# Kernel tuning notes

Hardware: AMD Instinct MI355X
Metric: run time of the kernel (lower is better)

Reference implementation:

```python
import jax, jax.numpy as jnp
import numpy as np

IN_C = 128
OUT_C = 128
N_SAMPLES = 9
N_HEADS = 8
HEAD_C = OUT_C // N_HEADS
SCALE = HEAD_C ** (-0.5)
B, FH, FW = 4, 128, 128


def setup_inputs() -> dict:
    key = jax.random.key(0)
    ks = jax.random.split(key, 8)
    w_std = IN_C ** (-0.5)
    q = jax.random.normal(ks[0], (B, IN_C, FH, FW), dtype=jnp.float32)
    kv = jax.random.normal(ks[1], (B, IN_C, N_SAMPLES, FH * FW), dtype=jnp.float32)
    Wq = jax.random.normal(ks[2], (OUT_C, IN_C), dtype=jnp.float32) * w_std
    bq = jax.random.normal(ks[3], (OUT_C,), dtype=jnp.float32) * 0.01
    Wk = jax.random.normal(ks[4], (OUT_C, IN_C), dtype=jnp.float32) * w_std
    bk = jax.random.normal(ks[5], (OUT_C,), dtype=jnp.float32) * 0.01
    Wv = jax.random.normal(ks[6], (OUT_C, IN_C), dtype=jnp.float32) * w_std
    bv = jax.random.normal(ks[7], (OUT_C,), dtype=jnp.float32) * 0.01
    return {"q": q, "kv": kv, "Wq": Wq, "bq": bq, "Wk": Wk, "bk": bk, "Wv": Wv, "bv": bv}


def reference(q, kv, Wq, bq, Wk, bk, Wv, bv):
    b, c, fh, fw = q.shape
    d = fh * fw
    # 1x1 conv projections == channel matmuls
    qp = (jnp.einsum('oc,bchw->bohw', Wq, q) + bq[None, :, None, None])
    qp = qp.reshape(b * N_HEADS, HEAD_C, d)                       # [bH, hc, d]
    kp = (jnp.einsum('oc,bcsd->bosd', Wk, kv) + bk[None, :, None, None])
    kp = kp.reshape(b * N_HEADS, HEAD_C, N_SAMPLES, d)            # [bH, hc, s, d]
    vp = (jnp.einsum('oc,bcsd->bosd', Wv, kv) + bv[None, :, None, None])
    vp = vp.reshape(b * N_HEADS, HEAD_C, N_SAMPLES, d)
    # per-pixel attention over n_samples keys
    attn = jnp.einsum('bcd,bcsd->bsd', qp, kp) * SCALE            # [bH, s, d]
    attn = jax.nn.softmax(attn, axis=1)
    out = jnp.einsum('bsd,bcsd->bcd', attn, vp)                   # [bH, hc, d]
    return out.reshape(b, OUT_C, fh, fw)
```

## Files before the change

### kernel.cpp

```cpp
#include <hip/hip_runtime.h>

#define D_PIX 16384
#define NSMP  9
#define TP    64
#define RS    136

typedef __attribute__((ext_vector_type(8))) short s16x8;
typedef __attribute__((ext_vector_type(4))) short s16x4;
typedef __attribute__((ext_vector_type(4))) float f32x4;

__device__ __forceinline__ short f2b(float f) {
    union { float f; unsigned u; } c; c.f = f;
    unsigned r = (c.u + 0x7FFFu + ((c.u >> 16) & 1u)) >> 16;
    return (short)r;
}

__global__ __launch_bounds__(256, 2)
void deform_attn_kernel(const float* __restrict__ q,
                        const float* __restrict__ kv,
                        const float* __restrict__ Wq,
                        const float* __restrict__ bq,
                        const float* __restrict__ Wk,
                        const float* __restrict__ bk,
                        const float* __restrict__ Wv,
                        const float* __restrict__ bv,
                        float* __restrict__ out)
{
    __shared__ short ldsb[2][TP * RS];

    const int tid  = threadIdx.x;
    const int bid  = blockIdx.x;
    const int b    = bid >> 8;
    const int px0  = (bid & 255) * TP;
    const int lane = tid & 63;
    const int w    = tid >> 6;
    const int r    = lane & 15;
    const int quad = lane >> 4;

    const int pxb = (tid & 7) * 8;
    const int chb = (tid >> 3) * 4;

    f32x4 pref[4][2];
    auto stage_load = [&](const float* base, int chstride) {
        #pragma unroll
        for (int j = 0; j < 4; ++j) {
            const float* p = base + (long)(chb + j) * chstride + pxb;
            pref[j][0] = *(const f32x4*)p;
            pref[j][1] = *(const f32x4*)(p + 4);
        }
    };
    auto stage_write = [&](short* buf) {
        #pragma unroll
        for (int i = 0; i < 8; ++i) {
            s16x4 v4 = { f2b(pref[0][i >> 2][i & 3]), f2b(pref[1][i >> 2][i & 3]),
                         f2b(pref[2][i >> 2][i & 3]), f2b(pref[3][i >> 2][i & 3]) };
            *(s16x4*)(buf + (pxb + i) * RS + chb) = v4;
        }
    };
    auto load_bfrags = [&](const short* buf, int n, s16x8* bfr) {
        #pragma unroll
        for (int ks = 0; ks < 4; ++ks)
            bfr[ks] = *(const s16x8*)(buf + (n * 16 + r) * RS + ks * 32 + quad * 8);
    };
    auto load_wfrag = [&](const float* W, int o, int ks) -> s16x8 {
        const float* p = W + o * 128 + ks * 32 + quad * 8;
        f32x4 a = *(const f32x4*)p;
        f32x4 c = *(const f32x4*)(p + 4);
        s16x8 f = { f2b(a[0]), f2b(a[1]), f2b(a[2]), f2b(a[3]),
                    f2b(c[0]), f2b(c[1]), f2b(c[2]), f2b(c[3]) };
        return f;
    };

    s16x8 wkF[2][4], wvF[2][4];
    float bkf[2][4], bvf[2][4], bqf[2][4];
    #pragma unroll
    for (int m = 0; m < 2; ++m) {
        const int o = (2 * w + m) * 16 + r;
        #pragma unroll
        for (int ks = 0; ks < 4; ++ks) {
            wkF[m][ks] = load_wfrag(Wk, o, ks);
            wvF[m][ks] = load_wfrag(Wv, o, ks);
        }
        const int ob = (2 * w + m) * 16 + quad * 4;
        #pragma unroll
        for (int rr = 0; rr < 4; ++rr) {
            bqf[m][rr] = bq[ob + rr];
            bkf[m][rr] = bk[ob + rr];
            bvf[m][rr] = bv[ob + rr];
        }
    }

    float qp[2][4][4];
    float oacc[2][4][4];
    float lsum[2][4];
    #pragma unroll
    for (int m = 0; m < 2; ++m)
        #pragma unroll
        for (int n = 0; n < 4; ++n) {
            lsum[m][n] = 0.f;
            #pragma unroll
            for (int rr = 0; rr < 4; ++rr) oacc[m][n][rr] = 0.f;
        }

    const float* qbase  = q  + (long)(b * 128) * D_PIX + px0;
    const float* kvbase = kv + (long)(b * 128) * NSMP * D_PIX + px0;

    stage_load(qbase, D_PIX);
    stage_write(ldsb[0]);
    __syncthreads();

    stage_load(kvbase, NSMP * D_PIX);
    {
        s16x8 wqF[2][4];
        #pragma unroll
        for (int m = 0; m < 2; ++m) {
            const int o = (2 * w + m) * 16 + r;
            #pragma unroll
            for (int ks = 0; ks < 4; ++ks)
                wqF[m][ks] = load_wfrag(Wq, o, ks);
        }
        #pragma unroll
        for (int n = 0; n < 4; ++n) {
            s16x8 bfr[4];
            load_bfrags(ldsb[0], n, bfr);
            #pragma unroll
            for (int m = 0; m < 2; ++m) {
                f32x4 acc = {0.f, 0.f, 0.f, 0.f};
                #pragma unroll
                for (int ks = 0; ks < 4; ++ks)
                    acc = __builtin_amdgcn_mfma_f32_16x16x32_bf16(wqF[m][ks], bfr[ks], acc, 0, 0, 0);
                #pragma unroll
                for (int rr = 0; rr < 4; ++rr) qp[m][n][rr] = acc[rr] + bqf[m][rr];
            }
        }
    }
    stage_write(ldsb[1]);
    __syncthreads();

    for (int s = 0; s < NSMP; ++s) {
        if (s < NSMP - 1) stage_load(kvbase + (s + 1) * D_PIX, NSMP * D_PIX);
        const short* buf = ldsb[(s + 1) & 1];
        #pragma unroll
        for (int n = 0; n < 4; ++n) {
            s16x8 bfr[4];
            load_bfrags(buf, n, bfr);
            #pragma unroll
            for (int m = 0; m < 2; ++m) {
                f32x4 kacc = {0.f, 0.f, 0.f, 0.f};
                f32x4 vacc = {0.f, 0.f, 0.f, 0.f};
                #pragma unroll
                for (int ks = 0; ks < 4; ++ks) {
                    kacc = __builtin_amdgcn_mfma_f32_16x16x32_bf16(wkF[m][ks], bfr[ks], kacc, 0, 0, 0);
                    vacc = __builtin_amdgcn_mfma_f32_16x16x32_bf16(wvF[m][ks], bfr[ks], vacc, 0, 0, 0);
                }
                float pf = 0.f;
                #pragma unroll
                for (int rr = 0; rr < 4; ++rr) pf += qp[m][n][rr] * (kacc[rr] + bkf[m][rr]);
                pf += __shfl_xor(pf, 16, 64);
                pf += __shfl_xor(pf, 32, 64);
                const float e = __expf(pf * 0.25f);
                lsum[m][n] += e;
                #pragma unroll
                for (int rr = 0; rr < 4; ++rr) oacc[m][n][rr] += e * (vacc[rr] + bvf[m][rr]);
            }
        }
        if (s < NSMP - 1) stage_write(ldsb[s & 1]);
        __syncthreads();
    }

    #pragma unroll
    for (int m = 0; m < 2; ++m) {
        #pragma unroll
        for (int n = 0; n < 4; ++n) {
            const float inv = 1.f / lsum[m][n];
            #pragma unroll
            for (int rr = 0; rr < 4; ++rr) {
                const int o = (2 * w + m) * 16 + quad * 4 + rr;
                out[(long)(b * 128 + o) * D_PIX + px0 + n * 16 + r] = oacc[m][n][rr] * inv;
            }
        }
    }
}

extern "C" void kernel_launch(void* const* d_in, const int* in_sizes, int n_in,
                              void* d_out, int out_size, void* d_ws, size_t ws_size,
                              hipStream_t stream) {
    const float* q  = (const float*)d_in[0];
    const float* kv = (const float*)d_in[1];
    const float* Wq = (const float*)d_in[2];
    const float* bq = (const float*)d_in[3];
    const float* Wk = (const float*)d_in[4];
    const float* bk = (const float*)d_in[5];
    const float* Wv = (const float*)d_in[6];
    const float* bv = (const float*)d_in[7];
    float* out = (float*)d_out;

    dim3 grid(1024);
    dim3 block(256);
    hipLaunchKernelGGL(deform_attn_kernel, grid, block, 0, stream,
                       q, kv, Wq, bq, Wk, bk, Wv, bv, out);
}
```

Baseline: 459.3 us.

## Use 512-thread blocks with one head per wave and fold biases algebraically

Doubles the block to 512 threads so each of eight waves owns a single 16-channel head, which halves per-thread register state (weights, accumulators) and the staging load per thread. The key bias is folded into a per-pixel constant q·bk computed once, and the value bias is added after normalisation because the softmax weights sum to one. The LDS row stride changes to 132 to suit the new 2-channel writes. The aim is higher occupancy and better latency hiding, at the cost of more waves contending at each barrier and a possible change in LDS bank conflicts.

```diff
diff --git a/kernel.cpp b/kernel.cpp
--- a/kernel.cpp
+++ b/kernel.cpp
@@ -3,10 +3,9 @@
 #define D_PIX 16384
 #define NSMP  9
 #define TP    64
-#define RS    136
+#define RS    132
 
 typedef __attribute__((ext_vector_type(8))) short s16x8;
-typedef __attribute__((ext_vector_type(4))) short s16x4;
 typedef __attribute__((ext_vector_type(4))) float f32x4;
 
 __device__ __forceinline__ short f2b(float f) {
@@ -15,7 +14,7 @@
     return (short)r;
 }
 
-__global__ __launch_bounds__(256, 2)
+__global__ __launch_bounds__(512, 4)
 void deform_attn_kernel(const float* __restrict__ q,
                         const float* __restrict__ kv,
                         const float* __restrict__ Wq,
@@ -38,12 +37,12 @@
     const int quad = lane >> 4;
 
     const int pxb = (tid & 7) * 8;
-    const int chb = (tid >> 3) * 4;
+    const int chb = (tid >> 3) * 2;
 
-    f32x4 pref[4][2];
-    auto stage_load = [&](const float* base, int chstride) {
+    f32x4 pref[2][2];
+    auto stage_load = [&](const float* base, long chstride) {
         #pragma unroll
-        for (int j = 0; j < 4; ++j) {
+        for (int j = 0; j < 2; ++j) {
             const float* p = base + (long)(chb + j) * chstride + pxb;
             pref[j][0] = *(const f32x4*)p;
             pref[j][1] = *(const f32x4*)(p + 4);
@@ -52,9 +51,8 @@
     auto stage_write = [&](short* buf) {
         #pragma unroll
         for (int i = 0; i < 8; ++i) {
-            s16x4 v4 = { f2b(pref[0][i >> 2][i & 3]), f2b(pref[1][i >> 2][i & 3]),
-                         f2b(pref[2][i >> 2][i & 3]), f2b(pref[3][i >> 2][i & 3]) };
-            *(s16x4*)(buf + (pxb + i) * RS + chb) = v4;
+            short2 v = { f2b(pref[0][i >> 2][i & 3]), f2b(pref[1][i >> 2][i & 3]) };
+            *(short2*)(buf + (pxb + i) * RS + chb) = v;
         }
     };
     auto load_bfrags = [&](const short* buf, int n, s16x8* bfr) {
@@ -71,113 +69,102 @@
         return f;
     };
 
-    s16x8 wkF[2][4], wvF[2][4];
-    float bkf[2][4], bvf[2][4], bqf[2][4];
-    #pragma unroll
-    for (int m = 0; m < 2; ++m) {
-        const int o = (2 * w + m) * 16 + r;
-        #pragma unroll
-        for (int ks = 0; ks < 4; ++ks) {
-            wkF[m][ks] = load_wfrag(Wk, o, ks);
-            wvF[m][ks] = load_wfrag(Wv, o, ks);
-        }
-        const int ob = (2 * w + m) * 16 + quad * 4;
-        #pragma unroll
-        for (int rr = 0; rr < 4; ++rr) {
-            bqf[m][rr] = bq[ob + rr];
-            bkf[m][rr] = bk[ob + rr];
-            bvf[m][rr] = bv[ob + rr];
-        }
-    }
-
-    float qp[2][4][4];
-    float oacc[2][4][4];
-    float lsum[2][4];
-    #pragma unroll
-    for (int m = 0; m < 2; ++m)
-        #pragma unroll
-        for (int n = 0; n < 4; ++n) {
-            lsum[m][n] = 0.f;
-            #pragma unroll
-            for (int rr = 0; rr < 4; ++rr) oacc[m][n][rr] = 0.f;
-        }
-
     const float* qbase  = q  + (long)(b * 128) * D_PIX + px0;
     const float* kvbase = kv + (long)(b * 128) * NSMP * D_PIX + px0;
+    const long   kvstr  = (long)NSMP * D_PIX;
 
     stage_load(qbase, D_PIX);
     stage_write(ldsb[0]);
     __syncthreads();
 
-    stage_load(kvbase, NSMP * D_PIX);
+    stage_load(kvbase, kvstr);
+    float qp[4][4];
     {
-        s16x8 wqF[2][4];
+        const int o = w * 16 + r;
+        s16x8 wqF[4];
         #pragma unroll
-        for (int m = 0; m < 2; ++m) {
-            const int o = (2 * w + m) * 16 + r;
-            #pragma unroll
-            for (int ks = 0; ks < 4; ++ks)
-                wqF[m][ks] = load_wfrag(Wq, o, ks);
-        }
+        for (int ks = 0; ks < 4; ++ks) wqF[ks] = load_wfrag(Wq, o, ks);
+        const int ob = w * 16 + quad * 4;
         #pragma unroll
         for (int n = 0; n < 4; ++n) {
             s16x8 bfr[4];
             load_bfrags(ldsb[0], n, bfr);
+            f32x4 acc = {0.f, 0.f, 0.f, 0.f};
             #pragma unroll
-            for (int m = 0; m < 2; ++m) {
-                f32x4 acc = {0.f, 0.f, 0.f, 0.f};
-                #pragma unroll
-                for (int ks = 0; ks < 4; ++ks)
-                    acc = __builtin_amdgcn_mfma_f32_16x16x32_bf16(wqF[m][ks], bfr[ks], acc, 0, 0, 0);
-                #pragma unroll
-                for (int rr = 0; rr < 4; ++rr) qp[m][n][rr] = acc[rr] + bqf[m][rr];
-            }
+            for (int ks = 0; ks < 4; ++ks)
+                acc = __builtin_amdgcn_mfma_f32_16x16x32_bf16(wqF[ks], bfr[ks], acc, 0, 0, 0);
+            #pragma unroll
+            for (int rr = 0; rr < 4; ++rr) qp[n][rr] = acc[rr] + bq[ob + rr];
         }
     }
     stage_write(ldsb[1]);
+
+    s16x8 wkF[4], wvF[4];
+    float bvf[4], qb[4];
+    {
+        const int o = w * 16 + r;
+        #pragma unroll
+        for (int ks = 0; ks < 4; ++ks) {
+            wkF[ks] = load_wfrag(Wk, o, ks);
+            wvF[ks] = load_wfrag(Wv, o, ks);
+        }
+        const int ob = w * 16 + quad * 4;
+        float bkf[4];
+        #pragma unroll
+        for (int rr = 0; rr < 4; ++rr) { bkf[rr] = bk[ob + rr]; bvf[rr] = bv[ob + rr]; }
+        #pragma unroll
+        for (int n = 0; n < 4; ++n) {
+            qb[n] = 0.f;
+            #pragma unroll
+            for (int rr = 0; rr < 4; ++rr) qb[n] += qp[n][rr] * bkf[rr];
+        }
+    }
+
+    float oacc[4][4];
+    float lsum[4];
+    #pragma unroll
+    for (int n = 0; n < 4; ++n) {
+        lsum[n] = 0.f;
+        #pragma unroll
+        for (int rr = 0; rr < 4; ++rr) oacc[n][rr] = 0.f;
+    }
     __syncthreads();
 
     for (int s = 0; s < NSMP; ++s) {
-        if (s < NSMP - 1) stage_load(kvbase + (s + 1) * D_PIX, NSMP * D_PIX);
+        if (s < NSMP - 1) stage_load(kvbase + (s + 1) * D_PIX, kvstr);
         const short* buf = ldsb[(s + 1) & 1];
         #pragma unroll
         for (int n = 0; n < 4; ++n) {
             s16x8 bfr[4];
             load_bfrags(buf, n, bfr);
+            f32x4 kacc = {0.f, 0.f, 0.f, 0.f};
+            f32x4 vacc = {0.f, 0.f, 0.f, 0.f};
             #pragma unroll
-            for (int m = 0; m < 2; ++m) {
-                f32x4 kacc = {0.f, 0.f, 0.f, 0.f};
-                f32x4 vacc = {0.f, 0.f, 0.f, 0.f};
-                #pragma unroll
-                for (int ks = 0; ks < 4; ++ks) {
-                    kacc = __builtin_amdgcn_mfma_f32_16x16x32_bf16(wkF[m][ks], bfr[ks], kacc, 0, 0, 0);
-                    vacc = __builtin_amdgcn_mfma_f32_16x16x32_bf16(wvF[m][ks], bfr[ks], vacc, 0, 0, 0);
-                }
-                float pf = 0.f;
-                #pragma unroll
-                for (int rr = 0; rr < 4; ++rr) pf += qp[m][n][rr] * (kacc[rr] + bkf[m][rr]);
-                pf += __shfl_xor(pf, 16, 64);
-                pf += __shfl_xor(pf, 32, 64);
-                const float e = __expf(pf * 0.25f);
-                lsum[m][n] += e;
-                #pragma unroll
-                for (int rr = 0; rr < 4; ++rr) oacc[m][n][rr] += e * (vacc[rr] + bvf[m][rr]);
+            for (int ks = 0; ks < 4; ++ks) {
+                kacc = __builtin_amdgcn_mfma_f32_16x16x32_bf16(wkF[ks], bfr[ks], kacc, 0, 0, 0);
+                vacc = __builtin_amdgcn_mfma_f32_16x16x32_bf16(wvF[ks], bfr[ks], vacc, 0, 0, 0);
             }
+            float pf = qb[n];
+            #pragma unroll
+            for (int rr = 0; rr < 4; ++rr) pf += qp[n][rr] * kacc[rr];
+            pf += __shfl_xor(pf, 16, 64);
+            pf += __shfl_xor(pf, 32, 64);
+            const float e = __expf(pf * 0.25f);
+            lsum[n] += e;
+            #pragma unroll
+            for (int rr = 0; rr < 4; ++rr) oacc[n][rr] += e * vacc[rr];
         }
         if (s < NSMP - 1) stage_write(ldsb[s & 1]);
         __syncthreads();
     }
 
     #pragma unroll
-    for (int m = 0; m < 2; ++m) {
+    for (int n = 0; n < 4; ++n) {
+        const float inv = 1.f / lsum[n];
         #pragma unroll
-        for (int n = 0; n < 4; ++n) {
-            const float inv = 1.f / lsum[m][n];
-            #pragma unroll
-            for (int rr = 0; rr < 4; ++rr) {
-                const int o = (2 * w + m) * 16 + quad * 4 + rr;
-                out[(long)(b * 128 + o) * D_PIX + px0 + n * 16 + r] = oacc[m][n][rr] * inv;
-            }
+        for (int rr = 0; rr < 4; ++rr) {
+            const int o = w * 16 + quad * 4 + rr;
+            out[(long)(b * 128 + o) * D_PIX + px0 + n * 16 + r] = oacc[n][rr] * inv + bvf[rr];
         }
     }
 }
@@ -196,7 +183,7 @@
     float* out = (float*)d_out;
 
     dim3 grid(1024);
-    dim3 block(256);
+    dim3 block(512);
     hipLaunchKernelGGL(deform_attn_kernel, grid, block, 0, stream,
                        q, kv, Wq, bq, Wk, bk, Wv, bv, out);
 }
```

After: 515.1 us. 1.12x slower.
